# Kernel optimization log

Measured on AMD Instinct MI355X. Metric: run time of the kernel, lower is better.

The kernel has to match this reference:

```python
import jax, jax.numpy as jnp
import numpy as np

EPS = 1e-6

def setup_inputs() -> dict:
    key = jax.random.key(0)
    k1, k2, k3 = jax.random.split(key, 3)
    N, L, S, H, D = 4, 4096, 4096, 8, 64
    queries = jax.random.normal(k1, (N, L, H, D), dtype=jnp.float32)
    keys = jax.random.normal(k2, (N, S, H, D), dtype=jnp.float32)
    values = jax.random.normal(k3, (N, S, H, D), dtype=jnp.float32)
    return {"queries": queries, "keys": keys, "values": values}

def _feature_map(x):
    # elu(x) + 1
    return jax.nn.elu(x) + 1.0

def reference(queries, keys, values):
    Q = _feature_map(queries)          # [N, L, H, D]
    K = _feature_map(keys)             # [N, S, H, D]
    v_length = values.shape[1]
    v = values / v_length              # [N, S, H, Dv]
    # KV outer-product sum over source positions: [N, H, D, Dv]
    KV = jnp.einsum('nshd,nshv->nhdv', K, v)
    # Normalizer: Q . sum_s K  -> [N, L, H]
    Z = 1.0 / (jnp.einsum('nlhd,nhd->nlh', Q, K.sum(axis=1)) + EPS)
    # Queried values: [N, L, H, Dv]
    out = jnp.einsum('nlhd,nhdv,nlh->nlhv', Q, KV, Z) * v_length
    return out
```

## Files before the change

kernel.cpp:

```cpp
#include <hip/hip_runtime.h>
#include <stdint.h>

#define NB   4
#define LQ   4096
#define SK   4096
#define NHD  8
#define DD   64
#define ROWSTRIDE (NHD * DD)
#define CH   32
#define SROWS (SK / CH)
#define KVSZ (DD * DD)
#define PART_STRIDE (KVSZ + DD)
#define NHTOT (NB * NHD)
#define LT   64
#define EPSF 1e-6f

typedef __attribute__((ext_vector_type(8))) short bf16x8;
typedef __attribute__((ext_vector_type(4))) float f32x4;

union FragU { uint32_t u[4]; bf16x8 v; };

__device__ __forceinline__ float fmap(float x) {
    return x > 0.f ? x + 1.f : __expf(x);
}

__device__ __forceinline__ void split8(const float* x, bf16x8& hi, bf16x8& lo) {
    FragU H, L;
#pragma unroll
    for (int p = 0; p < 4; ++p) {
        float a = x[2*p], b = x[2*p+1];
        uint32_t ua = __float_as_uint(a), ub = __float_as_uint(b);
        float ra = a - __uint_as_float(ua & 0xFFFF0000u);
        float rb = b - __uint_as_float(ub & 0xFFFF0000u);
        H.u[p] = (ua >> 16) | (ub & 0xFFFF0000u);
        L.u[p] = (__float_as_uint(ra) >> 16) | (__float_as_uint(rb) & 0xFFFF0000u);
    }
    hi = H.v; lo = L.v;
}

__global__ __launch_bounds__(256, 4) void k1_kv(const float* __restrict__ Kin,
                                                const float* __restrict__ Vin,
                                                float* __restrict__ part) {
    const int blk   = blockIdx.x;
    const int nh    = blk / CH;
    const int chunk = blk % CH;
    const int n = nh / NHD, h = nh % NHD;
    const int t = threadIdx.x;
    const int w = t >> 6, lane = t & 63;
    const int g = lane >> 4, r = lane & 15;
    const int wm = w & 1, wn = w >> 1;

    const size_t base = ((size_t)n * SK + (size_t)chunk * SROWS) * ROWSTRIDE
                        + (size_t)h * DD;

    const f32x4 zero4 = {0.f, 0.f, 0.f, 0.f};
    f32x4 acc[2][2] = {{zero4, zero4}, {zero4, zero4}};
    float ks[2] = {0.f, 0.f};

    for (int s0 = 0; s0 < SROWS; s0 += 32) {
        float xa[2][8], xb[2][8];
#pragma unroll
        for (int i = 0; i < 8; ++i) {
            const int soff = ((i & 4) << 2) + 4 * g + (i & 3);
            const size_t rowb = base + (size_t)(s0 + soff) * ROWSTRIDE;
#pragma unroll
            for (int mt = 0; mt < 2; ++mt)
                xa[mt][i] = Kin[rowb + (wm*2 + mt)*16 + r];
#pragma unroll
            for (int nt = 0; nt < 2; ++nt)
                xb[nt][i] = Vin[rowb + (wn*2 + nt)*16 + r];
        }
        bf16x8 ahi[2], alo[2], bhi[2], blo[2];
#pragma unroll
        for (int mt = 0; mt < 2; ++mt) {
#pragma unroll
            for (int i = 0; i < 8; ++i) xa[mt][i] = fmap(xa[mt][i]);
            if (wn == 0) {
#pragma unroll
                for (int i = 0; i < 8; ++i) ks[mt] += xa[mt][i];
            }
            split8(xa[mt], ahi[mt], alo[mt]);
        }
#pragma unroll
        for (int nt = 0; nt < 2; ++nt) split8(xb[nt], bhi[nt], blo[nt]);
#pragma unroll
        for (int mt = 0; mt < 2; ++mt)
#pragma unroll
            for (int nt = 0; nt < 2; ++nt) {
                acc[mt][nt] = __builtin_amdgcn_mfma_f32_16x16x32_bf16(
                                  ahi[mt], bhi[nt], acc[mt][nt], 0, 0, 0);
                acc[mt][nt] = __builtin_amdgcn_mfma_f32_16x16x32_bf16(
                                  alo[mt], bhi[nt], acc[mt][nt], 0, 0, 0);
                acc[mt][nt] = __builtin_amdgcn_mfma_f32_16x16x32_bf16(
                                  ahi[mt], blo[nt], acc[mt][nt], 0, 0, 0);
            }
    }

    float* pb = part + ((size_t)nh * CH + chunk) * PART_STRIDE;
#pragma unroll
    for (int mt = 0; mt < 2; ++mt) {
        const int dbase = (wm*2 + mt)*16 + 4*g;
#pragma unroll
        for (int nt = 0; nt < 2; ++nt) {
            const int e = (wn*2 + nt)*16 + r;
#pragma unroll
            for (int j = 0; j < 4; ++j)
                pb[(dbase + j) * DD + e] = acc[mt][nt][j];
        }
    }
    if (wn == 0) {
#pragma unroll
        for (int mt = 0; mt < 2; ++mt) {
            float v = ks[mt];
            v += __shfl_xor(v, 16);
            v += __shfl_xor(v, 32);
            if (lane < 16) pb[KVSZ + (wm*2 + mt)*16 + lane] = v;
        }
    }
}

__global__ __launch_bounds__(256) void k2_reduce(const float* __restrict__ part,
                                                 float* __restrict__ fin) {
    const int idx = blockIdx.x * 256 + threadIdx.x;
    if (idx >= NHTOT * PART_STRIDE) return;
    const int nh = idx / PART_STRIDE;
    const int j  = idx - nh * PART_STRIDE;
    const float* p = part + (size_t)nh * CH * PART_STRIDE + j;
    float s = 0.f;
#pragma unroll
    for (int cix = 0; cix < CH; ++cix) s += p[(size_t)cix * PART_STRIDE];
    fin[idx] = s;
}

#define KVSTR 72

__global__ __launch_bounds__(256) void k3_out(const float* __restrict__ Qin,
                                              const float* __restrict__ fin,
                                              float* __restrict__ out) {
    const int blk = blockIdx.x;
    const int nh  = blk >> 6;
    const int lc  = blk & 63;
    const int n = nh >> 3, h = nh & 7;
    const int t = threadIdx.x;
    const int w = t >> 6, lane = t & 63;
    const int g = lane >> 4, r = lane & 15;

    __shared__ __align__(16) short KThi[DD][KVSTR];
    __shared__ __align__(16) short KTlo[DD][KVSTR];
    __shared__ __align__(16) float Ksm[DD];

    const float* fb = fin + (size_t)nh * PART_STRIDE;
    {
        const int i0 = t * 16;
        const int d  = i0 >> 6;
        const int e0 = i0 & 63;
        float xs[16];
#pragma unroll
        for (int q = 0; q < 4; ++q) {
            const float4 x4 = *(const float4*)(fb + i0 + 4*q);
            xs[4*q+0] = x4.x; xs[4*q+1] = x4.y; xs[4*q+2] = x4.z; xs[4*q+3] = x4.w;
        }
        const int colb = (d & 32) | (d & 3) | (((d >> 4) & 1) << 2)
                         | (((d >> 2) & 3) << 3);
#pragma unroll
        for (int m = 0; m < 16; ++m) {
            const int e = e0 + m;
            const int col = colb ^ ((e & 3) << 3);
            const float x = xs[m];
            const uint32_t ux = __float_as_uint(x);
            const float lo = x - __uint_as_float(ux & 0xFFFF0000u);
            KThi[e][col] = (short)(ux >> 16);
            KTlo[e][col] = (short)(__float_as_uint(lo) >> 16);
        }
        if (t < DD) Ksm[t] = fb[KVSZ + t];
    }
    __syncthreads();

    const size_t qrow = (size_t)n * LQ + (size_t)lc * LT + w * 16 + r;
    const float* qp = Qin + qrow * ROWSTRIDE + (size_t)h * DD;

    const f32x4 zero4 = {0.f, 0.f, 0.f, 0.f};
    f32x4 acc[4] = {zero4, zero4, zero4, zero4};
    float z = 0.f;

#pragma unroll
    for (int kst = 0; kst < 2; ++kst) {
        const int kb = kst * 32;
        const float4 qa = *(const float4*)(qp + kb + 4*g);
        const float4 qb = *(const float4*)(qp + kb + 16 + 4*g);
        float qv[8] = {fmap(qa.x), fmap(qa.y), fmap(qa.z), fmap(qa.w),
                       fmap(qb.x), fmap(qb.y), fmap(qb.z), fmap(qb.w)};
        const float4 ka = *(const float4*)&Ksm[kb + 4*g];
        const float4 kc = *(const float4*)&Ksm[kb + 16 + 4*g];
        z += qv[0]*ka.x + qv[1]*ka.y + qv[2]*ka.z + qv[3]*ka.w
           + qv[4]*kc.x + qv[5]*kc.y + qv[6]*kc.z + qv[7]*kc.w;
        bf16x8 ahi, alo;
        split8(qv, ahi, alo);
        const int cswz = 8 * (g ^ (r & 3));
#pragma unroll
        for (int nt = 0; nt < 4; ++nt) {
            const int e = nt*16 + r;
            const bf16x8 bh = *(const bf16x8*)&KThi[e][kb + cswz];
            const bf16x8 bl = *(const bf16x8*)&KTlo[e][kb + cswz];
            acc[nt] = __builtin_amdgcn_mfma_f32_16x16x32_bf16(ahi, bh, acc[nt], 0,0,0);
            acc[nt] = __builtin_amdgcn_mfma_f32_16x16x32_bf16(alo, bh, acc[nt], 0,0,0);
            acc[nt] = __builtin_amdgcn_mfma_f32_16x16x32_bf16(ahi, bl, acc[nt], 0,0,0);
        }
    }

    z += __shfl_xor(z, 16);
    z += __shfl_xor(z, 32);

    const size_t obase0 = ((size_t)n * LQ + (size_t)lc * LT + w * 16) * ROWSTRIDE
                          + (size_t)h * DD;
#pragma unroll
    for (int j = 0; j < 4; ++j) {
        const float zj = __shfl(z, 4*g + j);
        const float zi = 1.f / (zj + EPSF);
        const size_t ob = obase0 + (size_t)(4*g + j) * ROWSTRIDE;
#pragma unroll
        for (int nt = 0; nt < 4; ++nt)
            out[ob + nt*16 + r] = acc[nt][j] * zi;
    }
}

extern "C" void kernel_launch(void* const* d_in, const int* in_sizes, int n_in,
                              void* d_out, int out_size, void* d_ws, size_t ws_size,
                              hipStream_t stream) {
    const float* Q = (const float*)d_in[0];
    const float* K = (const float*)d_in[1];
    const float* V = (const float*)d_in[2];
    float* out = (float*)d_out;

    float* ws   = (float*)d_ws;
    float* part = ws;
    float* fin  = ws + (size_t)NHTOT * CH * PART_STRIDE;

    k1_kv<<<NHTOT * CH, 256, 0, stream>>>(K, V, part);
    k2_reduce<<<(NHTOT * PART_STRIDE + 255) / 256, 256, 0, stream>>>(part, fin);
    k3_out<<<NHTOT * (LQ / LT), 256, 0, stream>>>(Q, fin, out);
}
```

Measured before the change: 150.0 us.

## Replace partial-sum reduce kernel with atomic accumulation and halve S chunks

Drops the separate reduction kernel and the per-chunk partial buffer. Each KV block now atomically adds its tile into a final buffer, which a small kernel zeroes first. The chunk count drops from 32 to 16, which lowers atomic contention but gives fewer, longer blocks. The launch-bounds occupancy hint is also removed. Float atomics make the summation order nondeterministic.

```diff
diff --git a/kernel.cpp b/kernel.cpp
--- a/kernel.cpp
+++ b/kernel.cpp
@@ -7,13 +7,14 @@
 #define NHD  8
 #define DD   64
 #define ROWSTRIDE (NHD * DD)
-#define CH   32
+#define CH   16
 #define SROWS (SK / CH)
 #define KVSZ (DD * DD)
 #define PART_STRIDE (KVSZ + DD)
 #define NHTOT (NB * NHD)
 #define LT   64
 #define EPSF 1e-6f
+#define FINSZ (NHTOT * PART_STRIDE)
 
 typedef __attribute__((ext_vector_type(8))) short bf16x8;
 typedef __attribute__((ext_vector_type(4))) float f32x4;
@@ -38,9 +39,16 @@
     hi = H.v; lo = L.v;
 }
 
-__global__ __launch_bounds__(256, 4) void k1_kv(const float* __restrict__ Kin,
-                                                const float* __restrict__ Vin,
-                                                float* __restrict__ part) {
+__global__ __launch_bounds__(256) void z0_zero(float* __restrict__ fin) {
+    const int i = (blockIdx.x * 256 + threadIdx.x) * 4;
+    if (i < FINSZ) {
+        *(float4*)(fin + i) = make_float4(0.f, 0.f, 0.f, 0.f);
+    }
+}
+
+__global__ __launch_bounds__(256) void k1_kv(const float* __restrict__ Kin,
+                                             const float* __restrict__ Vin,
+                                             float* __restrict__ fin) {
     const int blk   = blockIdx.x;
     const int nh    = blk / CH;
     const int chunk = blk % CH;
@@ -96,7 +104,7 @@
             }
     }
 
-    float* pb = part + ((size_t)nh * CH + chunk) * PART_STRIDE;
+    float* pb = fin + (size_t)nh * PART_STRIDE;
 #pragma unroll
     for (int mt = 0; mt < 2; ++mt) {
         const int dbase = (wm*2 + mt)*16 + 4*g;
@@ -105,7 +113,7 @@
             const int e = (wn*2 + nt)*16 + r;
 #pragma unroll
             for (int j = 0; j < 4; ++j)
-                pb[(dbase + j) * DD + e] = acc[mt][nt][j];
+                atomicAdd(pb + (dbase + j) * DD + e, acc[mt][nt][j]);
         }
     }
     if (wn == 0) {
@@ -114,22 +122,9 @@
             float v = ks[mt];
             v += __shfl_xor(v, 16);
             v += __shfl_xor(v, 32);
-            if (lane < 16) pb[KVSZ + (wm*2 + mt)*16 + lane] = v;
-        }
-    }
-}
-
-__global__ __launch_bounds__(256) void k2_reduce(const float* __restrict__ part,
-                                                 float* __restrict__ fin) {
-    const int idx = blockIdx.x * 256 + threadIdx.x;
-    if (idx >= NHTOT * PART_STRIDE) return;
-    const int nh = idx / PART_STRIDE;
-    const int j  = idx - nh * PART_STRIDE;
-    const float* p = part + (size_t)nh * CH * PART_STRIDE + j;
-    float s = 0.f;
-#pragma unroll
-    for (int cix = 0; cix < CH; ++cix) s += p[(size_t)cix * PART_STRIDE];
-    fin[idx] = s;
+            if (lane < 16) atomicAdd(pb + KVSZ + (wm*2 + mt)*16 + lane, v);
+        }
+    }
 }
 
 #define KVSTR 72
@@ -232,11 +227,9 @@
     const float* V = (const float*)d_in[2];
     float* out = (float*)d_out;
 
-    float* ws   = (float*)d_ws;
-    float* part = ws;
-    float* fin  = ws + (size_t)NHTOT * CH * PART_STRIDE;
-
-    k1_kv<<<NHTOT * CH, 256, 0, stream>>>(K, V, part);
-    k2_reduce<<<(NHTOT * PART_STRIDE + 255) / 256, 256, 0, stream>>>(part, fin);
+    float* fin = (float*)d_ws;
+
+    z0_zero<<<(FINSZ / 4 + 255) / 256, 256, 0, stream>>>(fin);
+    k1_kv<<<NHTOT * CH, 256, 0, stream>>>(K, V, fin);
     k3_out<<<NHTOT * (LQ / LT), 256, 0, stream>>>(Q, fin, out);
 }
```

After: 146.2 us. -2.6%, faster.

## Stage K/V tiles through LDS with coalesced float4 loads and prefetch in k1

Applied to the files above, without the earlier changes.

The KV accumulation kernel now loads K and V with coalesced float4 reads, applies the feature map and the bf16 hi/lo split once per element, and stores the split values in shared memory. MFMA operands are then read back as 128-bit LDS fragments. Previously each wave did scattered scalar global loads and redundant splits. The next tile is prefetched into registers while the current one computes, and the chunk count is halved so each block handles more rows and fewer partials need reducing. The cost is extra barriers and LDS traffic, plus reduced grid parallelism (512 blocks instead of 1024).

```diff
diff --git a/kernel.cpp b/kernel.cpp
--- a/kernel.cpp
+++ b/kernel.cpp
@@ -7,7 +7,7 @@
 #define NHD  8
 #define DD   64
 #define ROWSTRIDE (NHD * DD)
-#define CH   32
+#define CH   16
 #define SROWS (SK / CH)
 #define KVSZ (DD * DD)
 #define PART_STRIDE (KVSZ + DD)
@@ -18,7 +18,8 @@
 typedef __attribute__((ext_vector_type(8))) short bf16x8;
 typedef __attribute__((ext_vector_type(4))) float f32x4;
 
-union FragU { uint32_t u[4]; bf16x8 v; };
+union FragU  { uint32_t u[4]; bf16x8 v; };
+union Frag128 { uint4 q; bf16x8 v; };
 
 __device__ __forceinline__ float fmap(float x) {
     return x > 0.f ? x + 1.f : __expf(x);
@@ -38,9 +39,20 @@
     hi = H.v; lo = L.v;
 }
 
-__global__ __launch_bounds__(256, 4) void k1_kv(const float* __restrict__ Kin,
-                                                const float* __restrict__ Vin,
-                                                float* __restrict__ part) {
+__device__ __forceinline__ void split_pair(float a, float b,
+                                           uint32_t& hi, uint32_t& lo) {
+    uint32_t ua = __float_as_uint(a), ub = __float_as_uint(b);
+    float ra = a - __uint_as_float(ua & 0xFFFF0000u);
+    float rb = b - __uint_as_float(ub & 0xFFFF0000u);
+    hi = (ua >> 16) | (ub & 0xFFFF0000u);
+    lo = (__float_as_uint(ra) >> 16) | (__float_as_uint(rb) & 0xFFFF0000u);
+}
+
+#define PWORDS 20
+
+__global__ __launch_bounds__(256) void k1_kv(const float* __restrict__ Kin,
+                                             const float* __restrict__ Vin,
+                                             float* __restrict__ part) {
     const int blk   = blockIdx.x;
     const int nh    = blk / CH;
     const int chunk = blk % CH;
@@ -50,72 +62,104 @@
     const int g = lane >> 4, r = lane & 15;
     const int wm = w & 1, wn = w >> 1;
 
+    const int sp = t & 15;
+    const int c4 = t >> 4;
+
+    __shared__ __align__(16) uint32_t KHi[DD][PWORDS];
+    __shared__ __align__(16) uint32_t KLo[DD][PWORDS];
+    __shared__ __align__(16) uint32_t VHi[DD][PWORDS];
+    __shared__ __align__(16) uint32_t VLo[DD][PWORDS];
+
     const size_t base = ((size_t)n * SK + (size_t)chunk * SROWS) * ROWSTRIDE
                         + (size_t)h * DD;
+    const float* kp = Kin + base + (size_t)(2 * sp) * ROWSTRIDE + 4 * c4;
+    const float* vp = Vin + base + (size_t)(2 * sp) * ROWSTRIDE + 4 * c4;
 
     const f32x4 zero4 = {0.f, 0.f, 0.f, 0.f};
     f32x4 acc[2][2] = {{zero4, zero4}, {zero4, zero4}};
-    float ks[2] = {0.f, 0.f};
-
-    for (int s0 = 0; s0 < SROWS; s0 += 32) {
-        float xa[2][8], xb[2][8];
-#pragma unroll
-        for (int i = 0; i < 8; ++i) {
-            const int soff = ((i & 4) << 2) + 4 * g + (i & 3);
-            const size_t rowb = base + (size_t)(s0 + soff) * ROWSTRIDE;
-#pragma unroll
-            for (int mt = 0; mt < 2; ++mt)
-                xa[mt][i] = Kin[rowb + (wm*2 + mt)*16 + r];
-#pragma unroll
-            for (int nt = 0; nt < 2; ++nt)
-                xb[nt][i] = Vin[rowb + (wn*2 + nt)*16 + r];
-        }
-        bf16x8 ahi[2], alo[2], bhi[2], blo[2];
+    float ks[4] = {0.f, 0.f, 0.f, 0.f};
+
+    float4 k0 = *(const float4*)(kp);
+    float4 k1 = *(const float4*)(kp + ROWSTRIDE);
+    float4 v0 = *(const float4*)(vp);
+    float4 v1 = *(const float4*)(vp + ROWSTRIDE);
+
+#pragma unroll
+    for (int tile = 0; tile < SROWS / 32; ++tile) {
+        if (tile > 0) __syncthreads();
+
+        {
+            float kf0[4] = {fmap(k0.x), fmap(k0.y), fmap(k0.z), fmap(k0.w)};
+            float kf1[4] = {fmap(k1.x), fmap(k1.y), fmap(k1.z), fmap(k1.w)};
+            float vv0[4] = {v0.x, v0.y, v0.z, v0.w};
+            float vv1[4] = {v1.x, v1.y, v1.z, v1.w};
+#pragma unroll
+            for (int q = 0; q < 4; ++q) {
+                ks[q] += kf0[q] + kf1[q];
+                const int d = 4 * c4 + q;
+                uint32_t hi, lo;
+                split_pair(kf0[q], kf1[q], hi, lo);
+                KHi[d][sp] = hi; KLo[d][sp] = lo;
+                split_pair(vv0[q], vv1[q], hi, lo);
+                VHi[d][sp] = hi; VLo[d][sp] = lo;
+            }
+        }
+        __syncthreads();
+
+        if (tile < SROWS / 32 - 1) {
+            const size_t adv = (size_t)(tile + 1) * 32 * ROWSTRIDE;
+            k0 = *(const float4*)(kp + adv);
+            k1 = *(const float4*)(kp + adv + ROWSTRIDE);
+            v0 = *(const float4*)(vp + adv);
+            v1 = *(const float4*)(vp + adv + ROWSTRIDE);
+        }
+
+        Frag128 ahi[2], alo[2], bhi[2], blo[2];
 #pragma unroll
         for (int mt = 0; mt < 2; ++mt) {
-#pragma unroll
-            for (int i = 0; i < 8; ++i) xa[mt][i] = fmap(xa[mt][i]);
-            if (wn == 0) {
-#pragma unroll
-                for (int i = 0; i < 8; ++i) ks[mt] += xa[mt][i];
-            }
-            split8(xa[mt], ahi[mt], alo[mt]);
-        }
-#pragma unroll
-        for (int nt = 0; nt < 2; ++nt) split8(xb[nt], bhi[nt], blo[nt]);
+            const int d = (wm * 2 + mt) * 16 + r;
+            ahi[mt].q = *(const uint4*)&KHi[d][4 * g];
+            alo[mt].q = *(const uint4*)&KLo[d][4 * g];
+        }
+#pragma unroll
+        for (int nt = 0; nt < 2; ++nt) {
+            const int e = (wn * 2 + nt) * 16 + r;
+            bhi[nt].q = *(const uint4*)&VHi[e][4 * g];
+            blo[nt].q = *(const uint4*)&VLo[e][4 * g];
+        }
 #pragma unroll
         for (int mt = 0; mt < 2; ++mt)
 #pragma unroll
             for (int nt = 0; nt < 2; ++nt) {
                 acc[mt][nt] = __builtin_amdgcn_mfma_f32_16x16x32_bf16(
-                                  ahi[mt], bhi[nt], acc[mt][nt], 0, 0, 0);
+                                  ahi[mt].v, bhi[nt].v, acc[mt][nt], 0, 0, 0);
                 acc[mt][nt] = __builtin_amdgcn_mfma_f32_16x16x32_bf16(
-                                  alo[mt], bhi[nt], acc[mt][nt], 0, 0, 0);
+                                  alo[mt].v, bhi[nt].v, acc[mt][nt], 0, 0, 0);
                 acc[mt][nt] = __builtin_amdgcn_mfma_f32_16x16x32_bf16(
-                                  ahi[mt], blo[nt], acc[mt][nt], 0, 0, 0);
+                                  ahi[mt].v, blo[nt].v, acc[mt][nt], 0, 0, 0);
             }
     }
 
     float* pb = part + ((size_t)nh * CH + chunk) * PART_STRIDE;
 #pragma unroll
     for (int mt = 0; mt < 2; ++mt) {
-        const int dbase = (wm*2 + mt)*16 + 4*g;
+        const int dbase = (wm * 2 + mt) * 16 + 4 * g;
 #pragma unroll
         for (int nt = 0; nt < 2; ++nt) {
-            const int e = (wn*2 + nt)*16 + r;
+            const int e = (wn * 2 + nt) * 16 + r;
 #pragma unroll
             for (int j = 0; j < 4; ++j)
                 pb[(dbase + j) * DD + e] = acc[mt][nt][j];
         }
     }
-    if (wn == 0) {
-#pragma unroll
-        for (int mt = 0; mt < 2; ++mt) {
-            float v = ks[mt];
-            v += __shfl_xor(v, 16);
-            v += __shfl_xor(v, 32);
-            if (lane < 16) pb[KVSZ + (wm*2 + mt)*16 + lane] = v;
-        }
+
+#pragma unroll
+    for (int m = 1; m < 16; m <<= 1) {
+#pragma unroll
+        for (int q = 0; q < 4; ++q) ks[q] += __shfl_xor(ks[q], m);
+    }
+    if (sp == 0) {
+        *(float4*)(pb + KVSZ + 4 * c4) = make_float4(ks[0], ks[1], ks[2], ks[3]);
     }
 }
 
```

Result: faster. 144.9 us (-3.4%).
